# Optimization experiments

Measured on AMD Instinct MI355X. Metric: run time of the kernel, lower is better.

The kernel has to match this reference:

```python
import jax, jax.numpy as jnp
import numpy as np
import math

B, T, D = 2, 2048, 1024
H, HS = 16, 64  # n_heads, head_size; D == H*HS


def setup_inputs() -> dict:
    key = jax.random.key(0)
    k1, k2, k3 = jax.random.split(key, 3)
    x = jax.random.normal(k1, (B, T, D), dtype=jnp.float32)
    w_qkv = jax.random.normal(k2, (D, 3 * D), dtype=jnp.float32) * (1.0 / math.sqrt(D))
    b_qkv = jnp.zeros((3 * D,), dtype=jnp.float32)
    w_out = jax.random.normal(k3, (D, D), dtype=jnp.float32) * (1.0 / math.sqrt(D))
    b_out = jnp.zeros((D,), dtype=jnp.float32)
    return {"x": x, "w_qkv": w_qkv, "b_qkv": b_qkv, "w_out": w_out, "b_out": b_out}


def reference(x, w_qkv, b_qkv, w_out, b_out):
    b, t, d = x.shape
    qkv = x @ w_qkv + b_qkv                       # (B,T,3D)
    q, k, v = jnp.split(qkv, 3, axis=-1)
    # (B,T,D) -> (B,H,T,HS)
    q = q.reshape(b, t, H, HS).transpose(0, 2, 1, 3)
    k = k.reshape(b, t, H, HS).transpose(0, 2, 1, 3)
    v = v.reshape(b, t, H, HS).transpose(0, 2, 1, 3)
    scale = 1.0 / math.sqrt(HS)
    attn = jnp.einsum('bhqd,bhkd->bhqk', q, k) * scale  # (B,H,T,T)
    causal = jnp.tril(jnp.ones((t, t), dtype=bool))
    attn = jnp.where(causal[None, None], attn, -jnp.inf)
    attn = jax.nn.softmax(attn, axis=-1)
    o = jnp.einsum('bhqk,bhkd->bhqd', attn, v)          # (B,H,T,HS)
    o = o.transpose(0, 2, 1, 3).reshape(b, t, d)
    return o @ w_out + b_out
```

## Files before the change

kernel.cpp:

```cpp
#include <hip/hip_runtime.h>
#include <math.h>

#define B_  2
#define T_  2048
#define D_  1024
#define H_  16
#define HS_ 64
#define M_  (B_*T_)

typedef __bf16 bf16x8 __attribute__((ext_vector_type(8)));
typedef float  f32x4  __attribute__((ext_vector_type(4)));
typedef unsigned short u16;

static __device__ __forceinline__ u16 f2bf(float f) {
    __bf16 h = (__bf16)f;
    return *reinterpret_cast<u16*>(&h);
}

static __device__ __forceinline__ void glds16(const u16* g, u16* l) {
    __builtin_amdgcn_global_load_lds(
        (const __attribute__((address_space(1))) void*)g,
        (__attribute__((address_space(3))) void*)l, 16, 0, 0);
}

static __device__ __forceinline__ bf16x8 lds_chunk4(const u16* base, int row, int c) {
    return *reinterpret_cast<const bf16x8*>(base + (size_t)(row * 4 + (c ^ ((row >> 1) & 3))) * 8);
}

__global__ __launch_bounds__(256) void prep_kernel(
    const float* __restrict__ x, const float* __restrict__ w_qkv,
    const float* __restrict__ w_out,
    u16* __restrict__ Xb, u16* __restrict__ WqkvT, u16* __restrict__ WoutT)
{
    int bid = blockIdx.x;
    if (bid < 4096) {
        int i = (bid * 256 + threadIdx.x) * 4;
        float4 v = *reinterpret_cast<const float4*>(x + i);
        ushort4 o;
        o.x = f2bf(v.x); o.y = f2bf(v.y); o.z = f2bf(v.z); o.w = f2bf(v.w);
        *reinterpret_cast<ushort4*>(Xb + i) = o;
        return;
    }
    const float* in; u16* out; int C; int c0, r0;
    if (bid < 4096 + 3072) {
        int t = bid - 4096;
        in = w_qkv; out = WqkvT; C = 3 * D_;
        c0 = (t % 96) * 32; r0 = (t / 96) * 32;
    } else {
        int t = bid - 7168;
        in = w_out; out = WoutT; C = D_;
        c0 = (t & 31) * 32; r0 = (t >> 5) * 32;
    }
    __shared__ float tile[32][33];
    int tr = threadIdx.x >> 3, tc4 = (threadIdx.x & 7) * 4;
    float4 v = *reinterpret_cast<const float4*>(in + (size_t)(r0 + tr) * C + c0 + tc4);
    tile[tr][tc4+0] = v.x; tile[tr][tc4+1] = v.y;
    tile[tr][tc4+2] = v.z; tile[tr][tc4+3] = v.w;
    __syncthreads();
    ushort4 o;
    o.x = f2bf(tile[tc4+0][tr]); o.y = f2bf(tile[tc4+1][tr]);
    o.z = f2bf(tile[tc4+2][tr]); o.w = f2bf(tile[tc4+3][tr]);
    *reinterpret_cast<ushort4*>(out + (size_t)(c0 + tr) * D_ + r0 + tc4) = o;
}

template<int MODE>
__global__ __launch_bounds__(256) void gemm_bt(
    const u16* __restrict__ A, const u16* __restrict__ Bt,
    const float* __restrict__ bias,
    float* __restrict__ Cf,
    u16* __restrict__ Qb, u16* __restrict__ Kb, u16* __restrict__ Vt,
    int M, int N, int K)
{
    __shared__ u16 As[128 * 32];
    __shared__ u16 Bs[128 * 32];
    int tid  = threadIdx.x;
    int lane = tid & 63, wave = tid >> 6;
    int wm = wave >> 1, wn = wave & 1;
    int quad = lane >> 4, lr = lane & 15;
    int bm = blockIdx.x, bn = blockIdx.y;

    f32x4 acc[4][4] = {};

    const u16* Ab = A  + (size_t)(bm * 128) * K;
    const u16* Bb = Bt + (size_t)(bn * 128) * K;

    int r0 = tid >> 2,         c0 = (((tid) & 3) ^ ((tid >> 3) & 3)) * 8;
    int r1 = (tid + 256) >> 2, c1 = (((tid + 256) & 3) ^ (((tid + 256) >> 3) & 3)) * 8;

    for (int k0 = 0; k0 < K; k0 += 32) {
        __syncthreads();
        glds16(Ab + (size_t)r0 * K + k0 + c0, As + (size_t)tid * 8);
        glds16(Ab + (size_t)r1 * K + k0 + c1, As + (size_t)(tid + 256) * 8);
        glds16(Bb + (size_t)r0 * K + k0 + c0, Bs + (size_t)tid * 8);
        glds16(Bb + (size_t)r1 * K + k0 + c1, Bs + (size_t)(tid + 256) * 8);
        __syncthreads();
        bf16x8 af[4], bfr[4];
        #pragma unroll
        for (int i = 0; i < 4; ++i)
            af[i] = lds_chunk4(As, wm*64 + i*16 + lr, quad);
        #pragma unroll
        for (int j = 0; j < 4; ++j)
            bfr[j] = lds_chunk4(Bs, wn*64 + j*16 + lr, quad);
        #pragma unroll
        for (int i = 0; i < 4; ++i)
            #pragma unroll
            for (int j = 0; j < 4; ++j)
                acc[i][j] = __builtin_amdgcn_mfma_f32_16x16x32_bf16(af[i], bfr[j], acc[i][j], 0, 0, 0);
    }

    #pragma unroll
    for (int i = 0; i < 4; ++i) {
        int m0 = bm*128 + wm*64 + i*16 + quad*4;
        #pragma unroll
        for (int j = 0; j < 4; ++j) {
            int ncol = bn*128 + wn*64 + j*16 + lr;
            float bv = bias[ncol];
            float v4[4];
            #pragma unroll
            for (int r = 0; r < 4; ++r) v4[r] = acc[i][j][r] + bv;
            if (MODE == 1) {
                #pragma unroll
                for (int r = 0; r < 4; ++r)
                    Cf[(size_t)(m0 + r) * N + ncol] = v4[r];
            } else {
                int b = m0 >> 11, t0 = m0 & (T_ - 1);
                int s = ncol >> 10, rem = ncol & 1023;
                int h = rem >> 6, d = rem & 63;
                int bh = b * H_ + h;
                if (s == 0) {
                    #pragma unroll
                    for (int r = 0; r < 4; ++r)
                        Qb[((size_t)bh*T_ + t0 + r)*HS_ + d] = f2bf(v4[r] * 0.1803368801111244f);
                } else if (s == 1) {
                    #pragma unroll
                    for (int r = 0; r < 4; ++r)
                        Kb[((size_t)bh*T_ + t0 + r)*HS_ + d] = f2bf(v4[r]);
                } else {
                    ushort4 o;
                    o.x = f2bf(v4[0]); o.y = f2bf(v4[1]);
                    o.z = f2bf(v4[2]); o.w = f2bf(v4[3]);
                    *reinterpret_cast<ushort4*>(&Vt[((size_t)bh*HS_ + d)*T_ + t0]) = o;
                }
            }
        }
    }
}

__global__ __launch_bounds__(256) void attn_kernel(
    const u16* __restrict__ Qb, const u16* __restrict__ Kb,
    const u16* __restrict__ Vt, u16* __restrict__ Ob)
{
    __shared__ u16 Ks[64 * 64];
    __shared__ u16 Vs[64 * 64];
    __shared__ u16 Ps[4][16 * 64];

    int tid  = threadIdx.x;
    int lane = tid & 63, wave = tid >> 6;
    int quad = lane >> 4, lr = lane & 15;

    int lin = blockIdx.x;
    int bh  = (lin & 7) + 8 * ((lin >> 3) & 3);
    int idx = lin >> 5;
    int qt  = idx < 16 ? idx : 47 - idx;
    int qw  = qt * 64 + wave * 16;

    const u16* Qp = Qb + ((size_t)bh * T_ + qw) * HS_;
    bf16x8 qf[2];
    #pragma unroll
    for (int h2 = 0; h2 < 2; ++h2)
        qf[h2] = *reinterpret_cast<const bf16x8*>(Qp + lr*HS_ + h2*32 + quad*8);

    f32x4 Oa[4] = {};
    float lrow[4] = {0.f, 0.f, 0.f, 0.f};

    int e      = quad ^ (lr & 7);
    int rb0    = (lr * 8 + e) * 8;
    int rb1    = (lr * 8 + (e ^ 4)) * 8;
    int offw[4][4];
    #pragma unroll
    for (int nt = 0; nt < 4; ++nt)
        #pragma unroll
        for (int r = 0; r < 4; ++r) {
            int prow = quad*4 + r;
            offw[nt][r] = (prow*8 + ((nt*2 + (lr >> 3)) ^ (prow & 7)))*8 + (lr & 7);
        }
    u16* Psw = Ps[wave];

    int srow = tid >> 3;
    int scol = ((tid & 7) ^ (srow & 7)) * 8;
    const u16* kp0 = Kb + ((size_t)bh*T_ + srow     )*HS_ + scol;
    const u16* kp1 = Kb + ((size_t)bh*T_ + srow + 32)*HS_ + scol;
    const u16* vp0 = Vt + ((size_t)bh*HS_ + srow     )*T_ + scol;
    const u16* vp1 = Vt + ((size_t)bh*HS_ + srow + 32)*T_ + scol;

    bf16x8 kpre0 = *reinterpret_cast<const bf16x8*>(kp0);
    bf16x8 kpre1 = *reinterpret_cast<const bf16x8*>(kp1);
    bf16x8 vpre0 = *reinterpret_cast<const bf16x8*>(vp0);
    bf16x8 vpre1 = *reinterpret_cast<const bf16x8*>(vp1);

    for (int jt = 0; jt <= qt; ++jt) {
        __syncthreads();
        reinterpret_cast<bf16x8*>(Ks)[tid]       = kpre0;
        reinterpret_cast<bf16x8*>(Ks)[tid + 256] = kpre1;
        reinterpret_cast<bf16x8*>(Vs)[tid]       = vpre0;
        reinterpret_cast<bf16x8*>(Vs)[tid + 256] = vpre1;
        if (jt < qt) {
            kp0 += 64*HS_; kp1 += 64*HS_; vp0 += 64; vp1 += 64;
            kpre0 = *reinterpret_cast<const bf16x8*>(kp0);
            kpre1 = *reinterpret_cast<const bf16x8*>(kp1);
            vpre0 = *reinterpret_cast<const bf16x8*>(vp0);
            vpre1 = *reinterpret_cast<const bf16x8*>(vp1);
        }
        __syncthreads();

        f32x4 Sa[4] = {};
        #pragma unroll
        for (int nt = 0; nt < 4; ++nt) {
            bf16x8 bk0 = *reinterpret_cast<const bf16x8*>(Ks + rb0 + nt*1024);
            bf16x8 bk1 = *reinterpret_cast<const bf16x8*>(Ks + rb1 + nt*1024);
            Sa[nt] = __builtin_amdgcn_mfma_f32_16x16x32_bf16(qf[0], bk0, Sa[nt], 0, 0, 0);
            Sa[nt] = __builtin_amdgcn_mfma_f32_16x16x32_bf16(qf[1], bk1, Sa[nt], 0, 0, 0);
        }

        if (jt == qt) {
            int kb = jt * 64;
            #pragma unroll
            for (int nt = 0; nt < 4; ++nt)
                #pragma unroll
                for (int r = 0; r < 4; ++r) {
                    int kg = kb + nt*16 + lr;
                    int qg = qw + quad*4 + r;
                    if (kg > qg) Sa[nt][r] = -INFINITY;
                }
        }

        #pragma unroll
        for (int nt = 0; nt < 4; ++nt)
            #pragma unroll
            for (int r = 0; r < 4; ++r) {
                float pv = __builtin_amdgcn_exp2f(Sa[nt][r]);
                lrow[r] += pv;
                Psw[offw[nt][r]] = f2bf(pv);
            }

        #pragma unroll
        for (int kk = 0; kk < 2; ++kk) {
            int rb = kk ? rb1 : rb0;
            bf16x8 pa = *reinterpret_cast<const bf16x8*>(Psw + rb);
            #pragma unroll
            for (int nt = 0; nt < 4; ++nt) {
                bf16x8 vb = *reinterpret_cast<const bf16x8*>(Vs + rb + nt*1024);
                Oa[nt] = __builtin_amdgcn_mfma_f32_16x16x32_bf16(pa, vb, Oa[nt], 0, 0, 0);
            }
        }
    }

    int b = bh >> 4, h = bh & 15;
    #pragma unroll
    for (int r = 0; r < 4; ++r) {
        float s = lrow[r];
        #pragma unroll
        for (int off = 8; off >= 1; off >>= 1)
            s += __shfl_xor(s, off, 64);
        float inv = 1.f / s;
        int qg = qw + quad*4 + r;
        #pragma unroll
        for (int nt = 0; nt < 4; ++nt) {
            int d = nt*16 + lr;
            Ob[((size_t)b*T_ + qg)*D_ + h*HS_ + d] = f2bf(Oa[nt][r] * inv);
        }
    }
}

extern "C" void kernel_launch(void* const* d_in, const int* in_sizes, int n_in,
                              void* d_out, int out_size, void* d_ws, size_t ws_size,
                              hipStream_t stream) {
    (void)in_sizes; (void)n_in; (void)out_size; (void)ws_size;
    const float* x     = (const float*)d_in[0];
    const float* w_qkv = (const float*)d_in[1];
    const float* b_qkv = (const float*)d_in[2];
    const float* w_out = (const float*)d_in[3];
    const float* b_out = (const float*)d_in[4];
    float* out = (float*)d_out;

    char* ws = (char*)d_ws;
    u16* Xb    = (u16*)ws; ws += (size_t)M_ * D_ * 2;
    u16* WqkvT = (u16*)ws; ws += (size_t)3 * D_ * D_ * 2;
    u16* WoutT = (u16*)ws; ws += (size_t)D_ * D_ * 2;
    u16* Qb    = (u16*)ws; ws += (size_t)M_ * D_ * 2;
    u16* Kb    = (u16*)ws; ws += (size_t)M_ * D_ * 2;
    u16* Vt    = (u16*)ws; ws += (size_t)M_ * D_ * 2;
    u16* Ob    = (u16*)ws; ws += (size_t)M_ * D_ * 2;

    prep_kernel<<<8192, 256, 0, stream>>>(x, w_qkv, w_out, Xb, WqkvT, WoutT);
    gemm_bt<0><<<dim3(M_/128, 3*D_/128), 256, 0, stream>>>(
        Xb, WqkvT, b_qkv, nullptr, Qb, Kb, Vt, M_, 3*D_, D_);
    attn_kernel<<<1024, 256, 0, stream>>>(Qb, Kb, Vt, Ob);
    gemm_bt<1><<<dim3(M_/128, D_/128), 256, 0, stream>>>(
        Ob, WoutT, b_out, out, nullptr, nullptr, nullptr, M_, D_, D_);
}
```

Before: 183.0 us.

## Double-buffer GEMM with 64-wide K tiles and larger QKV tile

Replaces the single-buffered GEMM with a templated version. It uses 64-wide K steps, an XOR-swizzled LDS layout, and a two-stage double buffer so async global-to-LDS loads for step t+2 overlap the MFMA work of step t. Compute sections are wrapped in s_setprio raises. The QKV projection now uses 256x256 tiles with 512 threads to increase reuse per LDS load. The cost is much larger LDS use (about 128KB for the QKV variant) and more accumulator registers, which limits occupancy.

```diff
diff --git a/kernel.cpp b/kernel.cpp
--- a/kernel.cpp
+++ b/kernel.cpp
@@ -21,10 +21,6 @@
     __builtin_amdgcn_global_load_lds(
         (const __attribute__((address_space(1))) void*)g,
         (__attribute__((address_space(3))) void*)l, 16, 0, 0);
-}
-
-static __device__ __forceinline__ bf16x8 lds_chunk4(const u16* base, int row, int c) {
-    return *reinterpret_cast<const bf16x8*>(base + (size_t)(row * 4 + (c ^ ((row >> 1) & 3))) * 8);
 }
 
 __global__ __launch_bounds__(256) void prep_kernel(
@@ -63,57 +59,121 @@
     *reinterpret_cast<ushort4*>(out + (size_t)(c0 + tr) * D_ + r0 + tc4) = o;
 }
 
-template<int MODE>
-__global__ __launch_bounds__(256) void gemm_bt(
+template<int MODE, int BM, int BN, int WM, int WN, int NTH>
+__global__ __launch_bounds__(NTH, 2) void gemm_bt2(
     const u16* __restrict__ A, const u16* __restrict__ Bt,
     const float* __restrict__ bias,
     float* __restrict__ Cf,
     u16* __restrict__ Qb, u16* __restrict__ Kb, u16* __restrict__ Vt,
     int M, int N, int K)
 {
-    __shared__ u16 As[128 * 32];
-    __shared__ u16 Bs[128 * 32];
-    int tid  = threadIdx.x;
-    int lane = tid & 63, wave = tid >> 6;
-    int wm = wave >> 1, wn = wave & 1;
-    int quad = lane >> 4, lr = lane & 15;
-    int bm = blockIdx.x, bn = blockIdx.y;
-
-    f32x4 acc[4][4] = {};
-
-    const u16* Ab = A  + (size_t)(bm * 128) * K;
-    const u16* Bb = Bt + (size_t)(bn * 128) * K;
-
-    int r0 = tid >> 2,         c0 = (((tid) & 3) ^ ((tid >> 3) & 3)) * 8;
-    int r1 = (tid + 256) >> 2, c1 = (((tid + 256) & 3) ^ (((tid + 256) >> 3) & 3)) * 8;
-
-    for (int k0 = 0; k0 < K; k0 += 32) {
-        __syncthreads();
-        glds16(Ab + (size_t)r0 * K + k0 + c0, As + (size_t)tid * 8);
-        glds16(Ab + (size_t)r1 * K + k0 + c1, As + (size_t)(tid + 256) * 8);
-        glds16(Bb + (size_t)r0 * K + k0 + c0, Bs + (size_t)tid * 8);
-        glds16(Bb + (size_t)r1 * K + k0 + c1, Bs + (size_t)(tid + 256) * 8);
-        __syncthreads();
-        bf16x8 af[4], bfr[4];
-        #pragma unroll
-        for (int i = 0; i < 4; ++i)
-            af[i] = lds_chunk4(As, wm*64 + i*16 + lr, quad);
-        #pragma unroll
-        for (int j = 0; j < 4; ++j)
-            bfr[j] = lds_chunk4(Bs, wn*64 + j*16 + lr, quad);
-        #pragma unroll
-        for (int i = 0; i < 4; ++i)
-            #pragma unroll
-            for (int j = 0; j < 4; ++j)
-                acc[i][j] = __builtin_amdgcn_mfma_f32_16x16x32_bf16(af[i], bfr[j], acc[i][j], 0, 0, 0);
-    }
-
-    #pragma unroll
-    for (int i = 0; i < 4; ++i) {
-        int m0 = bm*128 + wm*64 + i*16 + quad*4;
-        #pragma unroll
-        for (int j = 0; j < 4; ++j) {
-            int ncol = bn*128 + wn*64 + j*16 + lr;
+    constexpr int MF  = BM / WM / 16;
+    constexpr int NF  = BN / WN / 16;
+    constexpr int NLA = BM * 8 / NTH;
+    constexpr int NLB = BN * 8 / NTH;
+
+    __shared__ u16 As[2][BM * 64];
+    __shared__ u16 Bs[2][BN * 64];
+
+    const int tid  = threadIdx.x;
+    const int lane = tid & 63, wave = tid >> 6;
+    const int wm = wave / WN, wn = wave % WN;
+    const int quad = lane >> 4, lr = lane & 15, x7 = lane & 7;
+    const int bm = blockIdx.x, bn = blockIdx.y;
+
+    const u16* Ab = A  + (size_t)(bm * BM) * K;
+    const u16* Bb = Bt + (size_t)(bn * BN) * K;
+
+    const u16* srcA[NLA]; int dA[NLA];
+    const u16* srcB[NLB]; int dB[NLB];
+    #pragma unroll
+    for (int j = 0; j < NLA; ++j) {
+        int ci = j * NTH + tid, r = ci >> 3, c = (ci & 7) ^ (r & 7);
+        srcA[j] = Ab + (size_t)r * K + c * 8;
+        dA[j] = ci * 8;
+    }
+    #pragma unroll
+    for (int j = 0; j < NLB; ++j) {
+        int ci = j * NTH + tid, r = ci >> 3, c = (ci & 7) ^ (r & 7);
+        srcB[j] = Bb + (size_t)r * K + c * 8;
+        dB[j] = ci * 8;
+    }
+
+    const int eA0 = (wm*(BM/WM) + lr)*64 + ((quad    ) ^ x7)*8;
+    const int eA1 = (wm*(BM/WM) + lr)*64 + ((quad | 4) ^ x7)*8;
+    const int eB0 = (wn*(BN/WN) + lr)*64 + ((quad    ) ^ x7)*8;
+    const int eB1 = (wn*(BN/WN) + lr)*64 + ((quad | 4) ^ x7)*8;
+
+    f32x4 acc[MF][NF] = {};
+    const int NT = K >> 6;
+
+    #pragma unroll
+    for (int j = 0; j < NLA; ++j) glds16(srcA[j], &As[0][dA[j]]);
+    #pragma unroll
+    for (int j = 0; j < NLB; ++j) glds16(srcB[j], &Bs[0][dB[j]]);
+    #pragma unroll
+    for (int j = 0; j < NLA; ++j) glds16(srcA[j] + 64, &As[1][dA[j]]);
+    #pragma unroll
+    for (int j = 0; j < NLB; ++j) glds16(srcB[j] + 64, &Bs[1][dB[j]]);
+    asm volatile("s_waitcnt vmcnt(8)" ::: "memory");
+    __builtin_amdgcn_s_barrier();
+
+    for (int t = 0; t < NT; ++t) {
+        const u16* Ac = As[t & 1];
+        const u16* Bc = Bs[t & 1];
+        bf16x8 a[MF], b[NF];
+
+        #pragma unroll
+        for (int i = 0; i < MF; ++i)
+            a[i] = *reinterpret_cast<const bf16x8*>(Ac + eA0 + i*1024);
+        #pragma unroll
+        for (int j = 0; j < NF; ++j)
+            b[j] = *reinterpret_cast<const bf16x8*>(Bc + eB0 + j*1024);
+        __builtin_amdgcn_s_setprio(1);
+        #pragma unroll
+        for (int i = 0; i < MF; ++i)
+            #pragma unroll
+            for (int j = 0; j < NF; ++j)
+                acc[i][j] = __builtin_amdgcn_mfma_f32_16x16x32_bf16(a[i], b[j], acc[i][j], 0, 0, 0);
+        __builtin_amdgcn_s_setprio(0);
+
+        #pragma unroll
+        for (int i = 0; i < MF; ++i)
+            a[i] = *reinterpret_cast<const bf16x8*>(Ac + eA1 + i*1024);
+        #pragma unroll
+        for (int j = 0; j < NF; ++j)
+            b[j] = *reinterpret_cast<const bf16x8*>(Bc + eB1 + j*1024);
+        asm volatile("s_waitcnt lgkmcnt(0)" ::: "memory");
+        __builtin_amdgcn_s_barrier();
+
+        if (t + 2 < NT) {
+            const int k0 = (t + 2) << 6;
+            u16* Ad = As[t & 1]; u16* Bd = Bs[t & 1];
+            #pragma unroll
+            for (int j = 0; j < NLA; ++j) glds16(srcA[j] + k0, Ad + dA[j]);
+            #pragma unroll
+            for (int j = 0; j < NLB; ++j) glds16(srcB[j] + k0, Bd + dB[j]);
+        }
+
+        __builtin_amdgcn_s_setprio(1);
+        #pragma unroll
+        for (int i = 0; i < MF; ++i)
+            #pragma unroll
+            for (int j = 0; j < NF; ++j)
+                acc[i][j] = __builtin_amdgcn_mfma_f32_16x16x32_bf16(a[i], b[j], acc[i][j], 0, 0, 0);
+        __builtin_amdgcn_s_setprio(0);
+
+        if (t + 2 < NT) { asm volatile("s_waitcnt vmcnt(8)" ::: "memory"); }
+        else           { asm volatile("s_waitcnt vmcnt(0)" ::: "memory"); }
+        __builtin_amdgcn_s_barrier();
+    }
+
+    #pragma unroll
+    for (int i = 0; i < MF; ++i) {
+        int m0 = bm*BM + wm*(BM/WM) + i*16 + quad*4;
+        #pragma unroll
+        for (int j = 0; j < NF; ++j) {
+            int ncol = bn*BN + wn*(BN/WN) + j*16 + lr;
             float bv = bias[ncol];
             float v4[4];
             #pragma unroll
@@ -123,10 +183,10 @@
                 for (int r = 0; r < 4; ++r)
                     Cf[(size_t)(m0 + r) * N + ncol] = v4[r];
             } else {
-                int b = m0 >> 11, t0 = m0 & (T_ - 1);
+                int bb = m0 >> 11, t0 = m0 & (T_ - 1);
                 int s = ncol >> 10, rem = ncol & 1023;
                 int h = rem >> 6, d = rem & 63;
-                int bh = b * H_ + h;
+                int bh = bb * H_ + h;
                 if (s == 0) {
                     #pragma unroll
                     for (int r = 0; r < 4; ++r)
@@ -293,9 +353,9 @@
     u16* Ob    = (u16*)ws; ws += (size_t)M_ * D_ * 2;
 
     prep_kernel<<<8192, 256, 0, stream>>>(x, w_qkv, w_out, Xb, WqkvT, WoutT);
-    gemm_bt<0><<<dim3(M_/128, 3*D_/128), 256, 0, stream>>>(
+    gemm_bt2<0, 256, 256, 2, 4, 512><<<dim3(M_/256, 3*D_/256), 512, 0, stream>>>(
         Xb, WqkvT, b_qkv, nullptr, Qb, Kb, Vt, M_, 3*D_, D_);
     attn_kernel<<<1024, 256, 0, stream>>>(Qb, Kb, Vt, Ob);
-    gemm_bt<1><<<dim3(M_/128, D_/128), 256, 0, stream>>>(
+    gemm_bt2<1, 128, 128, 2, 2, 256><<<dim3(M_/128, D_/128), 256, 0, stream>>>(
         Ob, WoutT, b_out, out, nullptr, nullptr, nullptr, M_, D_, D_);
 }
```

Result: faster. 175.7 us (-4.0%).
